# Optimization experiments

Measured on AMD Instinct MI355X. Metric: run time of the kernel, lower is better.

Reference implementation:

```python
import jax, jax.numpy as jnp
import numpy as np

# dims
B, N = 8, 64            # graphs, nodes per graph (equal-size ragged batch)
IN_DIM, EDGE_DIM = 16, 8
D, H = 128, 4
DH = D // H             # 32
L = 3                   # num_layers
FF = 4 * D              # 512
OUT = 1
SCALE = float(np.sqrt(DH))


def setup_inputs() -> dict:
    key = jax.random.key(0)
    ks = jax.random.split(key, 24)
    w = lambda k, s: jax.random.normal(k, s, jnp.float32) * 0.02
    return {
        'x': jax.random.normal(ks[0], (B, N, IN_DIM), jnp.float32),
        'edge_attr': jax.random.normal(ks[1], (B, N, N, EDGE_DIM), jnp.float32),
        'edge_mask': jax.random.bernoulli(ks[2], 0.2, (B, N, N)),
        # feature encoder (linear node + linear edge encoders, learned no-edge token)
        'node_W': w(ks[3], (IN_DIM, D)), 'node_b': jnp.zeros((D,), jnp.float32),
        'edge_W': w(ks[4], (EDGE_DIM, D)), 'edge_b': jnp.zeros((D,), jnp.float32),
        'no_edge': w(ks[5], (D,)),
        # per-layer edge-transformer params (stacked over L for lax.scan)
        'Wq': w(ks[6], (L, D, D)), 'Wk': w(ks[7], (L, D, D)),
        'Wv1': w(ks[8], (L, D, D)), 'Wv2': w(ks[9], (L, D, D)),
        'Wo': w(ks[10], (L, D, D)), 'bo': jnp.zeros((L, D), jnp.float32),
        'ln1_g': jnp.ones((L, D), jnp.float32), 'ln1_b': jnp.zeros((L, D), jnp.float32),
        'W1': w(ks[11], (L, D, FF)), 'b1': jnp.zeros((L, FF), jnp.float32),
        'W2': w(ks[12], (L, FF, D)), 'b2': jnp.zeros((L, D), jnp.float32),
        'ln2_g': jnp.ones((L, D), jnp.float32), 'ln2_b': jnp.zeros((L, D), jnp.float32),
        'Wout': w(ks[13], (D, OUT)), 'bout': jnp.zeros((OUT,), jnp.float32),
    }


def _ln(t, g, b):
    m = t.mean(-1, keepdims=True)
    v = t.var(-1, keepdims=True)
    return (t - m) * jax.lax.rsqrt(v + 1e-5) * g + b


def _forward(x, edge_attr, edge_mask, node_W, node_b, edge_W, edge_b, no_edge,
             Wq, Wk, Wv1, Wv2, Wo, bo, ln1_g, ln1_b, W1, b1, W2, b2,
             ln2_g, ln2_b, Wout, bout):
    # feature encoding: pair-token grid [B,N,N,D]
    node_emb = x @ node_W + node_b                       # [B,N,D]
    edge_emb = edge_attr @ edge_W + edge_b               # [B,N,N,D]
    tok = jnp.where(edge_mask[..., None], edge_emb, no_edge)
    eye = jnp.eye(N, dtype=bool)
    tok = jnp.where(eye[None, :, :, None], node_emb[:, :, None, :], tok)

    def heads(t, W):
        return (t @ W).reshape(B, N, N, H, DH)

    def layer(tok, p):
        wq, wk, wv1, wv2, wo, bo_, g1, b1_, w1, bf1, w2, bf2, g2, b2_ = p
        q = heads(tok, wq); k = heads(tok, wk)
        v1 = heads(tok, wv1); v2 = heads(tok, wv2)
        # triangular attention: token (i,j) attends over intermediate l
        s = jnp.einsum('bilhd,bljhd->bhilj', q, k) / SCALE   # [B,H,N,N,N]
        a = jax.nn.softmax(s, axis=3)                        # softmax over l
        o = jnp.einsum('bhilj,bilhd,bljhd->bijhd', a, v1, v2).reshape(B, N, N, D)
        tok = _ln(tok + o @ wo + bo_, g1, b1_)
        f = jax.nn.relu(tok @ w1 + bf1) @ w2 + bf2
        tok = _ln(tok + f, g2, b2_)
        return tok, None

    tok, _ = jax.lax.scan(
        layer, tok,
        (Wq, Wk, Wv1, Wv2, Wo, bo, ln1_g, ln1_b, W1, b1, W2, b2, ln2_g, ln2_b))

    diag = tok[:, jnp.arange(N), jnp.arange(N), :]           # node tokens [B,N,D]
    return diag @ Wout + bout                                 # [B,N,OUT]


def reference(x, edge_attr, edge_mask, node_W, node_b, edge_W, edge_b, no_edge,
              Wq, Wk, Wv1, Wv2, Wo, bo, ln1_g, ln1_b, W1, b1, W2, b2,
              ln2_g, ln2_b, Wout, bout):
    return _forward(x, edge_attr, edge_mask, node_W, node_b, edge_W, edge_b,
                    no_edge, Wq, Wk, Wv1, Wv2, Wo, bo, ln1_g, ln1_b,
                    W1, b1, W2, b2, ln2_g, ln2_b, Wout, bout)
```

## Files before the change

kernel.cpp:

```cpp
#include <hip/hip_runtime.h>

typedef unsigned short u16;
typedef __attribute__((ext_vector_type(8))) short bf16x8;
typedef __attribute__((ext_vector_type(4))) float f32x4;

#define INV_SCALE 0.17677669529663687f

static __device__ __forceinline__ float b2f(u16 u) {
    union { unsigned int i; float f; } v; v.i = ((unsigned int)u) << 16; return v.f;
}
static __device__ __forceinline__ u16 f2b(float f) {
    union { float f; unsigned int i; } v; v.f = f;
    unsigned int r = (v.i + 0x7FFFu + ((v.i >> 16) & 1u)) >> 16;
    return (u16)r;
}

#define NSEG 23
__device__ __constant__ int d_seg_off[NSEG + 1] = {
    0, 8192, 270336, 272384, 272512, 273536, 273664, 273792, 322944, 372096,
    421248, 470400, 519552, 519936, 520320, 520704, 717312, 718848, 915456,
    915840, 916224, 916608, 916736, 916744};
static const int h_seg_off[NSEG + 1] = {
    0, 8192, 270336, 272384, 272512, 273536, 273664, 273792, 322944, 372096,
    421248, 470400, 519552, 519936, 520320, 520704, 717312, 718848, 915456,
    915840, 916224, 916608, 916736, 916744};
#define ARENA_TOTAL 916744

struct ParamPtrs { const void* p[NSEG]; };

__global__ __launch_bounds__(256) void convert_params(ParamPtrs pp, u16* __restrict__ arena,
                                                      const void* __restrict__ mask,
                                                      int* __restrict__ mode) {
    if (blockIdx.x == 0) {
        __shared__ int f16, f32s, u8s;
        int tid = threadIdx.x;
        if (tid == 0) { f16 = 0; f32s = 0; u8s = 0; }
        __syncthreads();
        const u16* mu = (const u16*)mask;
        const unsigned int* mw = (const unsigned int*)mask;
        if (mu[2 * tid] == 0x3F80u) atomicOr(&f16, 1);
        if (mw[tid] == 0x3F800000u) atomicOr(&f32s, 1);
        if (mw[tid] > 1u) atomicOr(&u8s, 1);
        __syncthreads();
        if (tid == 0) mode[0] = f16 ? 0 : (f32s ? 3 : (u8s ? 1 : 2));
    }
    const unsigned int probe = ((const unsigned int*)pp.p[13])[0];
    const bool f32 = (probe == 0x3F800000u);
    for (int e = blockIdx.x * 256 + threadIdx.x; e < ARENA_TOTAL; e += gridDim.x * 256) {
        int k = 0;
        #pragma unroll
        for (int s2 = 1; s2 < NSEG; ++s2) if (e >= d_seg_off[s2]) k = s2;
        int local = e - d_seg_off[k];
        int src = local;
        if (k >= 7 && k <= 11) {
            int l = local >> 14, rem = local & 16383;
            int n = rem >> 7, kk = rem & 127;
            src = (l << 14) + kk * 128 + n;
        } else if (k == 15) {
            int l = local >> 16, rem = local & 65535;
            int n = rem >> 7, kk = rem & 127;
            src = (l << 16) + kk * 512 + n;
        } else if (k == 17) {
            int l = local >> 16, rem = local & 65535;
            int n = rem >> 9, kk = rem & 511;
            src = (l << 16) + kk * 128 + n;
        }
        u16 v;
        if (k == 22 && local >= 1) v = 0;
        else v = f32 ? f2b(((const float*)pp.p[k])[src]) : ((const u16*)pp.p[k])[src];
        arena[e] = v;
    }
}

__global__ __launch_bounds__(256) void assemble_kernel(
    const u16* __restrict__ x, const u16* __restrict__ ea,
    const void* __restrict__ mask, const int* __restrict__ modeptr,
    const u16* __restrict__ nodeW, const u16* __restrict__ nodeB,
    const u16* __restrict__ edgeW, const u16* __restrict__ edgeB, const u16* __restrict__ noedge,
    float* __restrict__ tokf, u16* __restrict__ tokb)
{
    const int md = modeptr[0];
    int g = blockIdx.x * 256 + threadIdx.x;
    int t = g >> 5, dq = g & 31, d0 = dq * 4;
    int b = t >> 12, i = (t >> 6) & 63, j = t & 63;
    float v[4];
    if (i == j) {
        #pragma unroll
        for (int c = 0; c < 4; c++) v[c] = b2f(nodeB[d0 + c]);
        #pragma unroll
        for (int e = 0; e < 16; e++) {
            float xe = b2f(x[(b * 64 + i) * 16 + e]);
            #pragma unroll
            for (int c = 0; c < 4; c++) v[c] += xe * b2f(nodeW[e * 128 + d0 + c]);
        }
    } else {
        bool edge;
        if (md == 0)      edge = ((const u16*)mask)[t] != 0;
        else if (md == 3) edge = ((const float*)mask)[t] != 0.0f;
        else if (md == 1) edge = ((const unsigned char*)mask)[t] != 0;
        else              edge = ((const unsigned int*)mask)[t] != 0;
        if (edge) {
            #pragma unroll
            for (int c = 0; c < 4; c++) v[c] = b2f(edgeB[d0 + c]);
            #pragma unroll
            for (int e = 0; e < 8; e++) {
                float ae = b2f(ea[t * 8 + e]);
                #pragma unroll
                for (int c = 0; c < 4; c++) v[c] += ae * b2f(edgeW[e * 128 + d0 + c]);
            }
        } else {
            #pragma unroll
            for (int c = 0; c < 4; c++) v[c] = b2f(noedge[d0 + c]);
        }
    }
    *(float4*)(tokf + (size_t)t * 128 + d0) = make_float4(v[0], v[1], v[2], v[3]);
    u16 pk[4];
    #pragma unroll
    for (int c = 0; c < 4; c++) pk[c] = f2b(v[c]);
    *(uint2*)(tokb + (size_t)t * 128 + d0) = *(uint2*)pk;
}

__global__ __launch_bounds__(256) void gemm_kernel(
    const u16* __restrict__ A, int lda,
    const u16* __restrict__ B0, const u16* __restrict__ B1,
    const u16* __restrict__ B2, const u16* __restrict__ B3,
    int ldbt, const u16* __restrict__ bias,
    int K, int mode,
    float* __restrict__ tokf,
    u16* __restrict__ qb, u16* __restrict__ kb, u16* __restrict__ v2b,
    const u16* __restrict__ lng, const u16* __restrict__ lnb, u16* __restrict__ tokbO)
{
    __shared__ __align__(16) u16 smem[64 * 72 + 128 * 72];
    u16* As = smem;
    u16* Bs = smem + 64 * 72;
    int tid = threadIdx.x;
    int m0 = blockIdx.x * 64;
    int by = blockIdx.y;
    const u16* Bp;
    if (mode == 3) { Bp = (by == 0) ? B0 : (by == 1) ? B1 : (by == 2) ? B2 : B3; }
    else { Bp = B0; }

    int w = tid >> 6, lane = tid & 63;
    int q = lane >> 4, r16 = lane & 15;
    int rw = (w >> 1) * 32, cw = (w & 1) * 64;

    f32x4 acc[2][4];
    #pragma unroll
    for (int mi = 0; mi < 2; mi++)
        #pragma unroll
        for (int ni = 0; ni < 4; ni++) acc[mi][ni] = (f32x4){0.f, 0.f, 0.f, 0.f};

    int nkt = K >> 6;
    for (int kt = 0; kt < nkt; ++kt) {
        int k0 = kt * 64;
        __syncthreads();
        #pragma unroll
        for (int it = 0; it < 2; ++it) {
            int idx = tid + it * 256;
            int row = idx >> 3, ch = idx & 7;
            uint4 d = *(const uint4*)(A + (size_t)(m0 + row) * lda + k0 + ch * 8);
            *(uint4*)&As[row * 72 + ch * 8] = d;
        }
        #pragma unroll
        for (int it = 0; it < 4; ++it) {
            int idx = tid + it * 256;
            int n = idx >> 3, ch = idx & 7;
            uint4 d = *(const uint4*)(Bp + (size_t)n * ldbt + k0 + ch * 8);
            int ch2 = ch ^ ((n >> 3) & 7);
            *(uint4*)&Bs[n * 72 + ch2 * 8] = d;
        }
        __syncthreads();
        #pragma unroll
        for (int ks = 0; ks < 2; ++ks) {
            bf16x8 fa[2], fb[4];
            #pragma unroll
            for (int mi = 0; mi < 2; mi++)
                fa[mi] = *(const bf16x8*)&As[(rw + mi * 16 + r16) * 72 + ks * 32 + q * 8];
            #pragma unroll
            for (int ni = 0; ni < 4; ni++) {
                int n = cw + ni * 16 + r16;
                int ch2 = (ks * 4 + q) ^ ((n >> 3) & 7);
                fb[ni] = *(const bf16x8*)&Bs[n * 72 + ch2 * 8];
            }
            #pragma unroll
            for (int mi = 0; mi < 2; mi++)
                #pragma unroll
                for (int ni = 0; ni < 4; ni++)
                    acc[mi][ni] = __builtin_amdgcn_mfma_f32_16x16x32_bf16(fa[mi], fb[ni], acc[mi][ni], 0, 0, 0);
        }
    }

    int bl = m0 >> 12, it0 = (m0 >> 6) & 63;
    __syncthreads();
    if (mode == 4) {
        float* cf  = (float*)smem;
        float* rsm = cf + 64 * 64;
        float* rqm = rsm + 128;
        int half = cw >> 6;
        #pragma unroll
        for (int ni = 0; ni < 4; ni++) {
            int col = cw + ni * 16 + r16;
            float bb = b2f(bias[col]);
            #pragma unroll
            for (int mi = 0; mi < 2; mi++)
                #pragma unroll
                for (int rr = 0; rr < 4; rr++) {
                    int r = rw + mi * 16 + q * 4 + rr;
                    acc[mi][ni][rr] += bb + tokf[(size_t)(m0 + r) * 128 + col];
                }
        }
        #pragma unroll
        for (int mi = 0; mi < 2; mi++)
            #pragma unroll
            for (int rr = 0; rr < 4; rr++) {
                float s = 0.f, sq = 0.f;
                #pragma unroll
                for (int ni = 0; ni < 4; ni++) { float t = acc[mi][ni][rr]; s += t; sq += t * t; }
                #pragma unroll
                for (int off = 1; off < 16; off <<= 1) {
                    s  += __shfl_xor(s,  off, 16);
                    sq += __shfl_xor(sq, off, 16);
                }
                if (r16 == 0) {
                    int r = rw + mi * 16 + q * 4 + rr;
                    rsm[half * 64 + r] = s;
                    rqm[half * 64 + r] = sq;
                }
            }
        __syncthreads();
        float gl[4], bv[4];
        #pragma unroll
        for (int ni = 0; ni < 4; ni++) {
            int col = cw + ni * 16 + r16;
            gl[ni] = b2f(lng[col]);
            bv[ni] = b2f(lnb[col]);
        }
        #pragma unroll
        for (int mi = 0; mi < 2; mi++)
            #pragma unroll
            for (int rr = 0; rr < 4; rr++) {
                int r = rw + mi * 16 + q * 4 + rr;
                float tot = rsm[r] + rsm[64 + r];
                float tq  = rqm[r] + rqm[64 + r];
                float mean = tot * 0.0078125f;
                float var  = tq * 0.0078125f - mean * mean;
                float rstd = rsqrtf(var + 1e-5f);
                #pragma unroll
                for (int ni = 0; ni < 4; ni++)
                    acc[mi][ni][rr] = (acc[mi][ni][rr] - mean) * rstd * gl[ni] + bv[ni];
            }
        #pragma unroll
        for (int hp = 0; hp < 2; ++hp) {
            __syncthreads();
            if (half == hp) {
                #pragma unroll
                for (int mi = 0; mi < 2; mi++)
                    #pragma unroll
                    for (int ni = 0; ni < 4; ni++) {
                        int colh = (cw & 63) + ni * 16 + r16;
                        int ch4 = colh >> 2, cl = colh & 3;
                        #pragma unroll
                        for (int rr = 0; rr < 4; rr++) {
                            int r = rw + mi * 16 + q * 4 + rr;
                            cf[r * 64 + (((ch4 ^ (r & 15)) << 2) | cl)] = acc[mi][ni][rr];
                        }
                    }
            }
            __syncthreads();
            #pragma unroll
            for (int it = 0; it < 4; ++it) {
                int idx = tid + it * 256;
                int r = idx >> 4, c4 = idx & 15;
                f32x4 v = *(const f32x4*)&cf[r * 64 + ((c4 ^ (r & 15)) << 2)];
                int col = hp * 64 + c4 * 4;
                *(f32x4*)(tokf + (size_t)(m0 + r) * 128 + col) = v;
                u16 pk[4];
                #pragma unroll
                for (int e = 0; e < 4; e++) pk[e] = f2b(v[e]);
                *(uint2*)(tokbO + (size_t)(m0 + r) * 128 + col) = *(uint2*)pk;
            }
        }
    } else if (mode == 3 && by == 2) {
        float* cf = (float*)smem;
        #pragma unroll
        for (int hp = 0; hp < 2; ++hp) {
            if (hp) __syncthreads();
            if ((cw >> 6) == hp) {
                #pragma unroll
                for (int mi = 0; mi < 2; mi++) {
                    #pragma unroll
                    for (int ni = 0; ni < 4; ni++) {
                        int colh = (cw & 63) + ni * 16 + r16;
                        int ch4 = colh >> 2, cl = colh & 3;
                        #pragma unroll
                        for (int rr = 0; rr < 4; rr++) {
                            int r = rw + mi * 16 + q * 4 + rr;
                            cf[r * 64 + (((ch4 ^ (r & 15)) << 2) | cl)] = acc[mi][ni][rr];
                        }
                    }
                }
            }
            __syncthreads();
            #pragma unroll
            for (int it = 0; it < 4; ++it) {
                int idx = tid + it * 256;
                int hh = idx >> 9, r = (idx >> 3) & 63, d4 = idx & 7;
                int colh = hh * 32 + d4 * 4;
                f32x4 v = *(const f32x4*)&cf[r * 64 + (((colh >> 2) ^ (r & 15)) << 2)];
                int h = hp * 2 + hh;
                *(f32x4*)&tokf[((((size_t)(bl * 4 + h)) * 64 + it0) * 64 + r) * 32 + d4 * 4] = v;
            }
        }
    } else {
        u16* cs = smem;
        #pragma unroll
        for (int mi = 0; mi < 2; mi++) {
            #pragma unroll
            for (int ni = 0; ni < 4; ni++) {
                int col = cw + ni * 16 + r16;
                int ch = col >> 3, cl = col & 7;
                #pragma unroll
                for (int rr = 0; rr < 4; rr++) {
                    int r = rw + mi * 16 + q * 4 + rr;
                    cs[r * 128 + (((ch ^ (r & 15)) << 3) | cl)] = f2b(acc[mi][ni][rr]);
                }
            }
        }
        __syncthreads();
        if (by == 0) {
            #pragma unroll
            for (int it = 0; it < 4; ++it) {
                int idx = tid + it * 256;
                int h = idx >> 8, r = (idx >> 2) & 63, d8 = idx & 3;
                int c8 = h * 4 + d8;
                uint4 d = *(const uint4*)&cs[r * 128 + ((c8 ^ (r & 15)) << 3)];
                *(uint4*)&qb[((((size_t)(bl * 4 + h)) * 64 + r) * 64 + it0) * 32 + d8 * 8] = d;
            }
        } else {
            u16* dp = (by == 1) ? kb : v2b;
            #pragma unroll
            for (int it = 0; it < 4; ++it) {
                int idx = tid + it * 256;
                int h = idx >> 8, r = (idx >> 2) & 63, d8 = idx & 3;
                int c8 = h * 4 + d8;
                uint4 d = *(const uint4*)&cs[r * 128 + ((c8 ^ (r & 15)) << 3)];
                *(uint4*)&dp[((((size_t)(bl * 4 + h)) * 64 + it0) * 64 + r) * 32 + d8 * 8] = d;
            }
        }
    }
}

__global__ __launch_bounds__(256) void ff_kernel(
    const u16* __restrict__ A,
    const u16* __restrict__ W1T, const u16* __restrict__ b1,
    const u16* __restrict__ W2T, const u16* __restrict__ b2,
    const u16* __restrict__ lng, const u16* __restrict__ lnb,
    float* __restrict__ tokf, u16* __restrict__ tokbO)
{
    __shared__ __align__(16) u16 smem[64 * 72 + 128 * 72];
    u16* As = smem;
    u16* Bs = smem + 64 * 72;
    int tid = threadIdx.x;
    int m0 = blockIdx.x * 64;
    int w = tid >> 6, lane = tid & 63;
    int q = lane >> 4, r16 = lane & 15;
    int rw = (w >> 1) * 32, cw = (w & 1) * 64;

    f32x4 acc2[2][4];
    #pragma unroll
    for (int mi = 0; mi < 2; mi++)
        #pragma unroll
        for (int ni = 0; ni < 4; ni++) acc2[mi][ni] = (f32x4){0.f, 0.f, 0.f, 0.f};

    for (int hs = 0; hs < 4; ++hs) {
        f32x4 acc1[2][4];
        #pragma unroll
        for (int mi = 0; mi < 2; mi++)
            #pragma unroll
            for (int ni = 0; ni < 4; ni++) acc1[mi][ni] = (f32x4){0.f, 0.f, 0.f, 0.f};
        #pragma unroll
        for (int kt = 0; kt < 2; ++kt) {
            int k0 = kt * 64;
            __syncthreads();
            #pragma unroll
            for (int it = 0; it < 2; ++it) {
                int idx = tid + it * 256;
                int row = idx >> 3, ch = idx & 7;
                uint4 d = *(const uint4*)(A + (size_t)(m0 + row) * 128 + k0 + ch * 8);
                *(uint4*)&As[row * 72 + ch * 8] = d;
            }
            #pragma unroll
            for (int it = 0; it < 4; ++it) {
                int idx = tid + it * 256;
                int n = idx >> 3, ch = idx & 7;
                uint4 d = *(const uint4*)(W1T + (size_t)(hs * 128 + n) * 128 + k0 + ch * 8);
                int ch2 = ch ^ ((n >> 3) & 7);
                *(uint4*)&Bs[n * 72 + ch2 * 8] = d;
            }
            __syncthreads();
            #pragma unroll
            for (int ks = 0; ks < 2; ++ks) {
                bf16x8 fa[2], fb[4];
                #pragma unroll
                for (int mi = 0; mi < 2; mi++)
                    fa[mi] = *(const bf16x8*)&As[(rw + mi * 16 + r16) * 72 + ks * 32 + q * 8];
                #pragma unroll
                for (int ni = 0; ni < 4; ni++) {
                    int n = cw + ni * 16 + r16;
                    int ch2 = (ks * 4 + q) ^ ((n >> 3) & 7);
                    fb[ni] = *(const bf16x8*)&Bs[n * 72 + ch2 * 8];
                }
                #pragma unroll
                for (int mi = 0; mi < 2; mi++)
                    #pragma unroll
                    for (int ni = 0; ni < 4; ni++)
                        acc1[mi][ni] = __builtin_amdgcn_mfma_f32_16x16x32_bf16(fa[mi], fb[ni], acc1[mi][ni], 0, 0, 0);
            }
        }
        #pragma unroll
        for (int half = 0; half < 2; ++half) {
            __syncthreads();
            if ((w & 1) == half) {
                #pragma unroll
                for (int mi = 0; mi < 2; mi++)
                    #pragma unroll
                    for (int ni = 0; ni < 4; ni++) {
                        int kl = ni * 16 + r16;
                        float bb = b2f(b1[hs * 128 + half * 64 + kl]);
                        #pragma unroll
                        for (int rr = 0; rr < 4; rr++) {
                            int row = rw + mi * 16 + q * 4 + rr;
                            As[row * 72 + kl] = f2b(fmaxf(acc1[mi][ni][rr] + bb, 0.f));
                        }
                    }
            }
            #pragma unroll
            for (int it = 0; it < 4; ++it) {
                int idx = tid + it * 256;
                int n = idx >> 3, ch = idx & 7;
                uint4 d = *(const uint4*)(W2T + (size_t)n * 512 + hs * 128 + half * 64 + ch * 8);
                int ch2 = ch ^ ((n >> 3) & 7);
                *(uint4*)&Bs[n * 72 + ch2 * 8] = d;
            }
            __syncthreads();
            #pragma unroll
            for (int ks = 0; ks < 2; ++ks) {
                bf16x8 fa[2], fb[4];
                #pragma unroll
                for (int mi = 0; mi < 2; mi++)
                    fa[mi] = *(const bf16x8*)&As[(rw + mi * 16 + r16) * 72 + ks * 32 + q * 8];
                #pragma unroll
                for (int ni = 0; ni < 4; ni++) {
                    int n = cw + ni * 16 + r16;
                    int ch2 = (ks * 4 + q) ^ ((n >> 3) & 7);
                    fb[ni] = *(const bf16x8*)&Bs[n * 72 + ch2 * 8];
                }
                #pragma unroll
                for (int mi = 0; mi < 2; mi++)
                    #pragma unroll
                    for (int ni = 0; ni < 4; ni++)
                        acc2[mi][ni] = __builtin_amdgcn_mfma_f32_16x16x32_bf16(fa[mi], fb[ni], acc2[mi][ni], 0, 0, 0);
            }
        }
    }

    __syncthreads();
    float* cf  = (float*)smem;
    float* rsm = cf + 64 * 64;
    float* rqm = rsm + 128;
    int half = cw >> 6;
    #pragma unroll
    for (int ni = 0; ni < 4; ni++) {
        int col = cw + ni * 16 + r16;
        float bb = b2f(b2[col]);
        #pragma unroll
        for (int mi = 0; mi < 2; mi++)
            #pragma unroll
            for (int rr = 0; rr < 4; rr++) {
                int r = rw + mi * 16 + q * 4 + rr;
                acc2[mi][ni][rr] += bb + tokf[(size_t)(m0 + r) * 128 + col];
            }
    }
    #pragma unroll
    for (int mi = 0; mi < 2; mi++)
        #pragma unroll
        for (int rr = 0; rr < 4; rr++) {
            float s = 0.f, sq = 0.f;
            #pragma unroll
            for (int ni = 0; ni < 4; ni++) { float t = acc2[mi][ni][rr]; s += t; sq += t * t; }
            #pragma unroll
            for (int off = 1; off < 16; off <<= 1) {
                s  += __shfl_xor(s,  off, 16);
                sq += __shfl_xor(sq, off, 16);
            }
            if (r16 == 0) {
                int r = rw + mi * 16 + q * 4 + rr;
                rsm[half * 64 + r] = s;
                rqm[half * 64 + r] = sq;
            }
        }
    __syncthreads();
    float gl[4], bv[4];
    #pragma unroll
    for (int ni = 0; ni < 4; ni++) {
        int col = cw + ni * 16 + r16;
        gl[ni] = b2f(lng[col]);
        bv[ni] = b2f(lnb[col]);
    }
    #pragma unroll
    for (int mi = 0; mi < 2; mi++)
        #pragma unroll
        for (int rr = 0; rr < 4; rr++) {
            int r = rw + mi * 16 + q * 4 + rr;
            float tot = rsm[r] + rsm[64 + r];
            float tq  = rqm[r] + rqm[64 + r];
            float mean = tot * 0.0078125f;
            float var  = tq * 0.0078125f - mean * mean;
            float rstd = rsqrtf(var + 1e-5f);
            #pragma unroll
            for (int ni = 0; ni < 4; ni++)
                acc2[mi][ni][rr] = (acc2[mi][ni][rr] - mean) * rstd * gl[ni] + bv[ni];
        }
    #pragma unroll
    for (int hp = 0; hp < 2; ++hp) {
        __syncthreads();
        if (half == hp) {
            #pragma unroll
            for (int mi = 0; mi < 2; mi++)
                #pragma unroll
                for (int ni = 0; ni < 4; ni++) {
                    int colh = (cw & 63) + ni * 16 + r16;
                    int ch4 = colh >> 2, cl = colh & 3;
                    #pragma unroll
                    for (int rr = 0; rr < 4; rr++) {
                        int r = rw + mi * 16 + q * 4 + rr;
                        cf[r * 64 + (((ch4 ^ (r & 15)) << 2) | cl)] = acc2[mi][ni][rr];
                    }
                }
        }
        __syncthreads();
        #pragma unroll
        for (int it = 0; it < 4; ++it) {
            int idx = tid + it * 256;
            int r = idx >> 4, c4 = idx & 15;
            f32x4 v = *(const f32x4*)&cf[r * 64 + ((c4 ^ (r & 15)) << 2)];
            int col = hp * 64 + c4 * 4;
            *(f32x4*)(tokf + (size_t)(m0 + r) * 128 + col) = v;
            u16 pk[4];
            #pragma unroll
            for (int e = 0; e < 4; e++) pk[e] = f2b(v[e]);
            *(uint2*)(tokbO + (size_t)(m0 + r) * 128 + col) = *(uint2*)pk;
        }
    }
}

__global__ __launch_bounds__(64) void attn_s_kernel(
    const u16* __restrict__ qb, const u16* __restrict__ kb, u16* __restrict__ s)
{
    __shared__ __align__(16) u16 sm[64 * 80];
    u16* qs  = sm;
    u16* ks_ = sm + 64 * 40;
    int g = blockIdx.x;
    int l = g & 63, bh = g >> 6;
    const u16* Q = qb + ((size_t)bh * 64 + l) * 2048;
    const u16* Kp = kb + ((size_t)bh * 64 + l) * 2048;
    int lane = threadIdx.x;
    #pragma unroll
    for (int it = 0; it < 4; ++it) {
        int idx = lane + it * 64;
        int row = idx >> 2, c4 = idx & 3;
        *(uint4*)&qs[row * 40 + c4 * 8] = *(const uint4*)(Q + row * 32 + c4 * 8);
        *(uint4*)&ks_[row * 40 + c4 * 8] = *(const uint4*)(Kp + row * 32 + c4 * 8);
    }
    __syncthreads();
    int q = lane >> 4, r16 = lane & 15;
    f32x4 acc[4][4];
    #pragma unroll
    for (int mi = 0; mi < 4; mi++)
        #pragma unroll
        for (int ni = 0; ni < 4; ni++) acc[mi][ni] = (f32x4){0.f, 0.f, 0.f, 0.f};
    bf16x8 fa[4], fb[4];
    #pragma unroll
    for (int mi = 0; mi < 4; mi++) fa[mi] = *(const bf16x8*)&qs[(mi * 16 + r16) * 40 + q * 8];
    #pragma unroll
    for (int ni = 0; ni < 4; ni++) fb[ni] = *(const bf16x8*)&ks_[(ni * 16 + r16) * 40 + q * 8];
    #pragma unroll
    for (int mi = 0; mi < 4; mi++)
        #pragma unroll
        for (int ni = 0; ni < 4; ni++)
            acc[mi][ni] = __builtin_amdgcn_mfma_f32_16x16x32_bf16(fa[mi], fb[ni], acc[mi][ni], 0, 0, 0);
    __syncthreads();
    u16* cs = sm;
    #pragma unroll
    for (int mi = 0; mi < 4; mi++)
        #pragma unroll
        for (int ni = 0; ni < 4; ni++)
            #pragma unroll
            for (int rr = 0; rr < 4; rr++)
                cs[(mi * 16 + q * 4 + rr) * 72 + ni * 16 + r16] = f2b(acc[mi][ni][rr] * INV_SCALE);
    __syncthreads();
    u16* sb = s + (size_t)bh * 262144 + l * 64;
    #pragma unroll
    for (int it = 0; it < 8; ++it) {
        int row = it * 8 + (lane >> 3);
        uint4 d = *(const uint4*)&cs[row * 72 + (lane & 7) * 8];
        *(uint4*)&sb[(size_t)row * 4096 + (lane & 7) * 8] = d;
    }
}

__global__ __launch_bounds__(256) void attn_o_kernel(
    const u16* __restrict__ a, const float* __restrict__ v1f, const u16* __restrict__ v2b,
    u16* __restrict__ ob)
{
    __shared__ __align__(16) float v2s[4 * 1152];
    __shared__ __align__(16) u16   as_[8 * 4 * 32];
    __shared__ __align__(16) float v1s[8 * 4 * 32];
    int bh = blockIdx.x;
    int i0 = blockIdx.y * 8;
    int jh = blockIdx.z;
    int bl = bh >> 2, h = bh & 3;
    int tid = threadIdx.x;
    int j32 = tid & 31;
    int ih = (tid >> 5) & 1;
    int dh = (tid >> 6) * 8;
    int jg = jh * 32 + j32;
    const u16*   v2base = v2b + (size_t)bh * 131072;
    const float* v1base = v1f + (size_t)bh * 131072 + (size_t)i0 * 2048;
    const u16*   abase  = a + (size_t)bh * 262144 + (size_t)i0 * 4096;

    int lz[2], jz[2], cz[2];
    #pragma unroll
    for (int it = 0; it < 2; ++it) {
        int idx = tid + it * 256;
        lz[it] = idx >> 7; jz[it] = (idx >> 2) & 31; cz[it] = idx & 3;
    }
    int ia = tid >> 5, la = (tid >> 3) & 3, jaq = tid & 7;
    int iv = tid >> 5, lv = (tid >> 3) & 3, dvq = (tid & 7) * 4;

    uint4 pv2[2]; uint2 pa; f32x4 pv1;

#define LOAD_CHUNK(l0_)                                                             \
    _Pragma("unroll")                                                               \
    for (int it = 0; it < 2; ++it)                                                  \
        pv2[it] = *(const uint4*)(v2base + ((size_t)((l0_) + lz[it]) * 64 + jh * 32 + jz[it]) * 32 + cz[it] * 8); \
    pa  = *(const uint2*)(abase + (size_t)ia * 4096 + ((l0_) + la) * 64 + jh * 32 + jaq * 4); \
    pv1 = *(const f32x4*)(v1base + (size_t)iv * 2048 + ((l0_) + lv) * 32 + dvq);

#define STORE_CHUNK()                                                               \
    _Pragma("unroll")                                                               \
    for (int it = 0; it < 2; ++it) {                                                \
        const u16* ds = (const u16*)&pv2[it];                                       \
        float* dst = &v2s[lz[it] * 1152 + jz[it] * 36 + cz[it] * 8];                \
        _Pragma("unroll")                                                           \
        for (int e = 0; e < 8; e++) dst[e] = b2f(ds[e]);                            \
    }                                                                               \
    *(uint2*)&as_[ia * 128 + la * 32 + jaq * 4] = pa;                               \
    *(f32x4*)&v1s[iv * 128 + lv * 32 + dvq] = pv1;

    float acc[4][8];
    float Z[4];
    #pragma unroll
    for (int i = 0; i < 4; i++) {
        Z[i] = 0.f;
        #pragma unroll
        for (int e = 0; e < 8; e++) acc[i][e] = 0.f;
    }

    LOAD_CHUNK(0);
    for (int ch = 0; ch < 16; ++ch) {
        if (ch) __syncthreads();
        STORE_CHUNK();
        if (ch + 1 < 16) LOAD_CHUNK((ch + 1) * 4);
        __syncthreads();
        #pragma unroll
        for (int lc = 0; lc < 4; ++lc) {
            const float* vp = &v2s[lc * 1152 + j32 * 36 + dh];
            float v2r[8];
            *(f32x4*)&v2r[0] = *(const f32x4*)vp;
            *(f32x4*)&v2r[4] = *(const f32x4*)(vp + 4);
            #pragma unroll
            for (int ii = 0; ii < 4; ++ii) {
                int iL = ih * 4 + ii;
                float sv = b2f(as_[iL * 128 + lc * 32 + j32]);
                float av = __expf(sv);
                Z[ii] += av;
                const float* v1p = &v1s[iL * 128 + lc * 32 + dh];
                #pragma unroll
                for (int e = 0; e < 8; e++)
                    acc[ii][e] += (av * v1p[e]) * v2r[e];
            }
        }
    }
#undef LOAD_CHUNK
#undef STORE_CHUNK

    #pragma unroll
    for (int ii = 0; ii < 4; ++ii) {
        int iL = ih * 4 + ii;
        float sc = 1.0f / Z[ii];
        u16 tmp[8];
        #pragma unroll
        for (int e = 0; e < 8; e++) tmp[e] = f2b(acc[ii][e] * sc);
        *(uint4*)(ob + ((size_t)(bl * 64 + i0 + iL) * 64 + jg) * 128 + h * 32 + dh) = *(uint4*)tmp;
    }
}

__global__ __launch_bounds__(256) void out_kernel(
    const float* __restrict__ tokf, const u16* __restrict__ Wout, const u16* __restrict__ bout,
    float* __restrict__ out)
{
    int g = blockIdx.x * 256 + threadIdx.x;
    int b = g >> 6, i = g & 63;
    const float* p = tokf + ((size_t)(b * 64 + i) * 64 + i) * 128;
    float s = b2f(bout[0]);
    #pragma unroll
    for (int d = 0; d < 128; d++) s += p[d] * b2f(Wout[d]);
    out[g] = s;
}

extern "C" void kernel_launch(void* const* d_in, const int* in_sizes, int n_in,
                              void* d_out, int out_size, void* d_ws, size_t ws_size,
                              hipStream_t stream) {
    const void* mask = d_in[2];
    ParamPtrs pp;
    for (int k = 0; k < NSEG; ++k) pp.p[k] = d_in[k < 2 ? k : k + 1];

    char* ws = (char*)d_ws;
    u16* arena = (u16*)ws;
    #define AP(k) ((const u16*)ws + h_seg_off[k])
    int*   mmode = (int*)(ws + 1835008);
    float* tokf  = (float*)(ws + 2097152);
    u16*   tokb  = (u16*)(ws + 18874368);
    const size_t base = 27262976;
    const size_t MB = 1048576ULL;

    int NB = 8;
    while (NB > 1 && base + (size_t)NB * 7 * MB > ws_size) NB >>= 1;

    u16*   qb  = (u16*)(ws + base);
    u16*   kb  = (u16*)(ws + base + (size_t)NB * MB);
    u16*   v2b = (u16*)(ws + base + (size_t)NB * 2 * MB);
    float* v1f = (float*)(ws + base + (size_t)NB * 3 * MB);
    u16*   sb  = (u16*)(ws + base + (size_t)NB * 5 * MB);
    u16*   ob  = qb;

    convert_params<<<1024, 256, 0, stream>>>(pp, arena, mask, mmode);
    assemble_kernel<<<4096, 256, 0, stream>>>(AP(0), AP(1), mask, mmode,
                                              AP(2), AP(3), AP(4), AP(5), AP(6), tokf, tokb);

    for (int l = 0; l < 3; ++l) {
        const u16* Wq_l  = AP(7)  + l * 16384;
        const u16* Wk_l  = AP(8)  + l * 16384;
        const u16* Wv1_l = AP(9)  + l * 16384;
        const u16* Wv2_l = AP(10) + l * 16384;
        const u16* Wo_l  = AP(11) + l * 16384;
        const u16* bo_l  = AP(12) + l * 128;
        const u16* g1_l  = AP(13) + l * 128;
        const u16* be1_l = AP(14) + l * 128;
        const u16* W1_l  = AP(15) + l * 65536;
        const u16* b1_l  = AP(16) + l * 512;
        const u16* W2_l  = AP(17) + l * 65536;
        const u16* b2_l  = AP(18) + l * 128;
        const u16* g2_l  = AP(19) + l * 128;
        const u16* be2_l = AP(20) + l * 128;

        for (int r = 0; r < 8 / NB; ++r) {
            size_t rowOff = (size_t)r * NB * 4096;
            gemm_kernel<<<dim3(NB * 64, 4), 256, 0, stream>>>(
                tokb + rowOff * 128, 128, Wq_l, Wk_l, Wv1_l, Wv2_l,
                128, (const u16*)0, 128, 3, v1f, qb, kb, v2b,
                (const u16*)0, (const u16*)0, (u16*)0);
            attn_s_kernel<<<NB * 256, 64, 0, stream>>>(qb, kb, sb);
            attn_o_kernel<<<dim3(NB * 4, 8, 2), 256, 0, stream>>>(sb, v1f, v2b, ob);
            gemm_kernel<<<dim3(NB * 64, 1), 256, 0, stream>>>(
                ob, 128, Wo_l, (const u16*)0, (const u16*)0, (const u16*)0,
                128, bo_l, 128, 4, tokf + rowOff * 128,
                (u16*)0, (u16*)0, (u16*)0,
                g1_l, be1_l, tokb + rowOff * 128);
        }
        ff_kernel<<<512, 256, 0, stream>>>(tokb, W1_l, b1_l, W2_l, b2_l,
                                           g2_l, be2_l, tokf, tokb);
    }
    out_kernel<<<2, 256, 0, stream>>>(tokf, AP(21), AP(22), (float*)d_out);
}
```

Baseline: 413.0 us.

## Fuse triangular attention score computation into the attention output kernel

Removes the separate attn_s kernel that wrote bf16 scores to global memory. Scores are now computed per chunk inside attn_o with MFMA over Q/K tiles staged in shared memory, kept in fp32 and consumed immediately. This drops a launch and a round trip of the score tensor through global memory. In exchange each block recomputes scores redundantly across the two j-halves, adds another barrier per chunk, uses more shared memory, and ob moves to a separate buffer.

```diff
diff --git a/kernel.cpp b/kernel.cpp
--- a/kernel.cpp
+++ b/kernel.cpp
@@ -554,67 +554,16 @@
     }
 }
 
-__global__ __launch_bounds__(64) void attn_s_kernel(
-    const u16* __restrict__ qb, const u16* __restrict__ kb, u16* __restrict__ s)
-{
-    __shared__ __align__(16) u16 sm[64 * 80];
-    u16* qs  = sm;
-    u16* ks_ = sm + 64 * 40;
-    int g = blockIdx.x;
-    int l = g & 63, bh = g >> 6;
-    const u16* Q = qb + ((size_t)bh * 64 + l) * 2048;
-    const u16* Kp = kb + ((size_t)bh * 64 + l) * 2048;
-    int lane = threadIdx.x;
-    #pragma unroll
-    for (int it = 0; it < 4; ++it) {
-        int idx = lane + it * 64;
-        int row = idx >> 2, c4 = idx & 3;
-        *(uint4*)&qs[row * 40 + c4 * 8] = *(const uint4*)(Q + row * 32 + c4 * 8);
-        *(uint4*)&ks_[row * 40 + c4 * 8] = *(const uint4*)(Kp + row * 32 + c4 * 8);
-    }
-    __syncthreads();
-    int q = lane >> 4, r16 = lane & 15;
-    f32x4 acc[4][4];
-    #pragma unroll
-    for (int mi = 0; mi < 4; mi++)
-        #pragma unroll
-        for (int ni = 0; ni < 4; ni++) acc[mi][ni] = (f32x4){0.f, 0.f, 0.f, 0.f};
-    bf16x8 fa[4], fb[4];
-    #pragma unroll
-    for (int mi = 0; mi < 4; mi++) fa[mi] = *(const bf16x8*)&qs[(mi * 16 + r16) * 40 + q * 8];
-    #pragma unroll
-    for (int ni = 0; ni < 4; ni++) fb[ni] = *(const bf16x8*)&ks_[(ni * 16 + r16) * 40 + q * 8];
-    #pragma unroll
-    for (int mi = 0; mi < 4; mi++)
-        #pragma unroll
-        for (int ni = 0; ni < 4; ni++)
-            acc[mi][ni] = __builtin_amdgcn_mfma_f32_16x16x32_bf16(fa[mi], fb[ni], acc[mi][ni], 0, 0, 0);
-    __syncthreads();
-    u16* cs = sm;
-    #pragma unroll
-    for (int mi = 0; mi < 4; mi++)
-        #pragma unroll
-        for (int ni = 0; ni < 4; ni++)
-            #pragma unroll
-            for (int rr = 0; rr < 4; rr++)
-                cs[(mi * 16 + q * 4 + rr) * 72 + ni * 16 + r16] = f2b(acc[mi][ni][rr] * INV_SCALE);
-    __syncthreads();
-    u16* sb = s + (size_t)bh * 262144 + l * 64;
-    #pragma unroll
-    for (int it = 0; it < 8; ++it) {
-        int row = it * 8 + (lane >> 3);
-        uint4 d = *(const uint4*)&cs[row * 72 + (lane & 7) * 8];
-        *(uint4*)&sb[(size_t)row * 4096 + (lane & 7) * 8] = d;
-    }
-}
-
 __global__ __launch_bounds__(256) void attn_o_kernel(
-    const u16* __restrict__ a, const float* __restrict__ v1f, const u16* __restrict__ v2b,
+    const u16* __restrict__ qb, const u16* __restrict__ kb,
+    const float* __restrict__ v1f, const u16* __restrict__ v2b,
     u16* __restrict__ ob)
 {
     __shared__ __align__(16) float v2s[4 * 1152];
-    __shared__ __align__(16) u16   as_[8 * 4 * 32];
+    __shared__ __align__(16) u16   ks_[4 * 1280];
+    __shared__ __align__(16) u16   qs_[4 * 640];
     __shared__ __align__(16) float v1s[8 * 4 * 32];
+    __shared__ __align__(16) float st[4 * 256];
     int bh = blockIdx.x;
     int i0 = blockIdx.y * 8;
     int jh = blockIdx.z;
@@ -622,11 +571,19 @@
     int tid = threadIdx.x;
     int j32 = tid & 31;
     int ih = (tid >> 5) & 1;
-    int dh = (tid >> 6) * 8;
-    int jg = jh * 32 + j32;
+    int w = tid >> 6;
+    int dh = w * 8;
+    int lane = tid & 63;
+    int q = lane >> 4, r16 = lane & 15;
+    const u16*   qbase  = qb  + (size_t)bh * 131072;
+    const u16*   kbase  = kb  + (size_t)bh * 131072;
     const u16*   v2base = v2b + (size_t)bh * 131072;
     const float* v1base = v1f + (size_t)bh * 131072 + (size_t)i0 * 2048;
-    const u16*   abase  = a + (size_t)bh * 262144 + (size_t)i0 * 4096;
+
+    for (int idx = tid; idx < 4 * 8 * 40; idx += 256) {
+        int l = idx / 320, rr = (idx / 40) & 7, c = idx % 40;
+        qs_[l * 640 + (8 + rr) * 40 + c] = 0;
+    }
 
     int lz[2], jz[2], cz[2];
     #pragma unroll
@@ -634,27 +591,30 @@
         int idx = tid + it * 256;
         lz[it] = idx >> 7; jz[it] = (idx >> 2) & 31; cz[it] = idx & 3;
     }
-    int ia = tid >> 5, la = (tid >> 3) & 3, jaq = tid & 7;
+    int lq = tid >> 6, iq = (tid >> 3) & 7, cq = tid & 7;
     int iv = tid >> 5, lv = (tid >> 3) & 3, dvq = (tid & 7) * 4;
 
-    uint4 pv2[2]; uint2 pa; f32x4 pv1;
+    uint4 pk[2], pv2[2]; uint2 pq; f32x4 pv1;
 
 #define LOAD_CHUNK(l0_)                                                             \
     _Pragma("unroll")                                                               \
-    for (int it = 0; it < 2; ++it)                                                  \
+    for (int it = 0; it < 2; ++it) {                                                \
+        pk[it]  = *(const uint4*)(kbase  + ((size_t)((l0_) + lz[it]) * 64 + jh * 32 + jz[it]) * 32 + cz[it] * 8); \
         pv2[it] = *(const uint4*)(v2base + ((size_t)((l0_) + lz[it]) * 64 + jh * 32 + jz[it]) * 32 + cz[it] * 8); \
-    pa  = *(const uint2*)(abase + (size_t)ia * 4096 + ((l0_) + la) * 64 + jh * 32 + jaq * 4); \
+    }                                                                               \
+    pq  = *(const uint2*)(qbase + (size_t)((l0_) + lq) * 2048 + (i0 + iq) * 32 + cq * 4); \
     pv1 = *(const f32x4*)(v1base + (size_t)iv * 2048 + ((l0_) + lv) * 32 + dvq);
 
 #define STORE_CHUNK()                                                               \
     _Pragma("unroll")                                                               \
     for (int it = 0; it < 2; ++it) {                                                \
+        *(uint4*)&ks_[lz[it] * 1280 + jz[it] * 40 + cz[it] * 8] = pk[it];           \
         const u16* ds = (const u16*)&pv2[it];                                       \
         float* dst = &v2s[lz[it] * 1152 + jz[it] * 36 + cz[it] * 8];                \
         _Pragma("unroll")                                                           \
         for (int e = 0; e < 8; e++) dst[e] = b2f(ds[e]);                            \
     }                                                                               \
-    *(uint2*)&as_[ia * 128 + la * 32 + jaq * 4] = pa;                               \
+    *(uint2*)&qs_[lq * 640 + iq * 40 + cq * 4] = pq;                                \
     *(f32x4*)&v1s[iv * 128 + lv * 32 + dvq] = pv1;
 
     float acc[4][8];
@@ -672,6 +632,23 @@
         STORE_CHUNK();
         if (ch + 1 < 16) LOAD_CHUNK((ch + 1) * 4);
         __syncthreads();
+        {
+            bf16x8 fa  = *(const bf16x8*)&qs_[w * 640 + r16 * 40 + q * 8];
+            bf16x8 fb0 = *(const bf16x8*)&ks_[w * 1280 + r16 * 40 + q * 8];
+            bf16x8 fb1 = *(const bf16x8*)&ks_[w * 1280 + (16 + r16) * 40 + q * 8];
+            f32x4 s0 = (f32x4){0.f, 0.f, 0.f, 0.f};
+            f32x4 s1 = (f32x4){0.f, 0.f, 0.f, 0.f};
+            s0 = __builtin_amdgcn_mfma_f32_16x16x32_bf16(fa, fb0, s0, 0, 0, 0);
+            s1 = __builtin_amdgcn_mfma_f32_16x16x32_bf16(fa, fb1, s1, 0, 0, 0);
+            if (q < 2) {
+                #pragma unroll
+                for (int rr = 0; rr < 4; rr++) {
+                    st[w * 256 + (q * 4 + rr) * 32 + r16]      = s0[rr] * INV_SCALE;
+                    st[w * 256 + (q * 4 + rr) * 32 + 16 + r16] = s1[rr] * INV_SCALE;
+                }
+            }
+        }
+        __syncthreads();
         #pragma unroll
         for (int lc = 0; lc < 4; ++lc) {
             const float* vp = &v2s[lc * 1152 + j32 * 36 + dh];
@@ -681,7 +658,7 @@
             #pragma unroll
             for (int ii = 0; ii < 4; ++ii) {
                 int iL = ih * 4 + ii;
-                float sv = b2f(as_[iL * 128 + lc * 32 + j32]);
+                float sv = st[lc * 256 + iL * 32 + j32];
                 float av = __expf(sv);
                 Z[ii] += av;
                 const float* v1p = &v1s[iL * 128 + lc * 32 + dh];
@@ -694,6 +671,7 @@
 #undef LOAD_CHUNK
 #undef STORE_CHUNK
 
+    int jg = jh * 32 + j32;
     #pragma unroll
     for (int ii = 0; ii < 4; ++ii) {
         int iL = ih * 4 + ii;
@@ -735,14 +713,13 @@
     const size_t MB = 1048576ULL;
 
     int NB = 8;
-    while (NB > 1 && base + (size_t)NB * 7 * MB > ws_size) NB >>= 1;
+    while (NB > 1 && base + (size_t)NB * 6 * MB > ws_size) NB >>= 1;
 
     u16*   qb  = (u16*)(ws + base);
     u16*   kb  = (u16*)(ws + base + (size_t)NB * MB);
     u16*   v2b = (u16*)(ws + base + (size_t)NB * 2 * MB);
     float* v1f = (float*)(ws + base + (size_t)NB * 3 * MB);
-    u16*   sb  = (u16*)(ws + base + (size_t)NB * 5 * MB);
-    u16*   ob  = qb;
+    u16*   ob  = (u16*)(ws + base + (size_t)NB * 5 * MB);
 
     convert_params<<<1024, 256, 0, stream>>>(pp, arena, mask, mmode);
     assemble_kernel<<<4096, 256, 0, stream>>>(AP(0), AP(1), mask, mmode,
@@ -770,8 +747,7 @@
                 tokb + rowOff * 128, 128, Wq_l, Wk_l, Wv1_l, Wv2_l,
                 128, (const u16*)0, 128, 3, v1f, qb, kb, v2b,
                 (const u16*)0, (const u16*)0, (u16*)0);
-            attn_s_kernel<<<NB * 256, 64, 0, stream>>>(qb, kb, sb);
-            attn_o_kernel<<<dim3(NB * 4, 8, 2), 256, 0, stream>>>(sb, v1f, v2b, ob);
+            attn_o_kernel<<<dim3(NB * 4, 8, 2), 256, 0, stream>>>(qb, kb, v1f, v2b, ob);
             gemm_kernel<<<dim3(NB * 64, 1), 256, 0, stream>>>(
                 ob, 128, Wo_l, (const u16*)0, (const u16*)0, (const u16*)0,
                 128, bo_l, 128, 4, tokf + rowOff * 128,
```

After: 445.4 us. +7.9%, slower.
